# Kernel tuning notes

Hardware: AMD Instinct MI355X
Metric: run time of the kernel (lower is better)

## Reference

```python
import jax, jax.numpy as jnp
import numpy as np

B, H, O, T = 256, 1024, 512, 128


def setup_inputs() -> dict:
    key = jax.random.key(0)
    ks = jax.random.split(key, 7)
    s = 1.0 / np.sqrt(H)
    return {
        "C": jax.random.normal(ks[0], (B, H), jnp.float32),
        "W_ih": jax.random.normal(ks[1], (4 * H, H), jnp.float32) * s,
        "W_hh": jax.random.normal(ks[2], (4 * H, H), jnp.float32) * s,
        "b_ih": jax.random.normal(ks[3], (4 * H,), jnp.float32) * s,
        "b_hh": jax.random.normal(ks[4], (4 * H,), jnp.float32) * s,
        "W_lin": jax.random.normal(ks[5], (O, H), jnp.float32) * s,
        "b_lin": jax.random.normal(ks[6], (O,), jnp.float32) * s,
        "max_seq_len": T,
    }


def reference(C, W_ih, W_hh, b_ih, b_hh, W_lin, b_lin, max_seq_len):
    batch, hid = C.shape
    # Input is the same C at every timestep -> precompute input projection once.
    x_proj = C @ W_ih.T + b_ih + b_hh  # [B, 4H]

    def step(carry, _):
        h, c = carry
        gates = x_proj + h @ W_hh.T  # [B, 4H]
        i, f, g, o = jnp.split(gates, 4, axis=-1)  # torch gate order i,f,g,o
        i = jax.nn.sigmoid(i)
        f = jax.nn.sigmoid(f)
        g = jnp.tanh(g)
        o = jax.nn.sigmoid(o)
        c = f * c + i * g
        h = o * jnp.tanh(c)
        y = h @ W_lin.T + b_lin  # [B, O]
        return (h, c), y

    h0 = jnp.zeros((batch, hid), C.dtype)
    c0 = jnp.zeros((batch, hid), C.dtype)
    _, ys = jax.lax.scan(step, (h0, c0), None, length=max_seq_len)
    return ys  # [T, B, O]
```

## Files before the change

kernel.cpp:

```cpp
#include <hip/hip_runtime.h>

typedef _Float16 f16;
typedef _Float16 f16x4 __attribute__((ext_vector_type(4)));
typedef _Float16 f16x8 __attribute__((ext_vector_type(8)));
typedef float f32x2 __attribute__((ext_vector_type(2)));
typedef float f32x4 __attribute__((ext_vector_type(4)));

#define LSTM_B 256
#define LSTM_H 1024
#define LSTM_O 512
#define LSTM_T 128
#define GATES 4096


__global__ void cvt4_kernel(const float4* __restrict__ src, f16x4* __restrict__ dst, int n4) {
  int i = blockIdx.x * blockDim.x + threadIdx.x;
  int st = gridDim.x * blockDim.x;
  for (; i < n4; i += st) {
    float4 v = src[i];
    f16x4 o; o[0] = (f16)v.x; o[1] = (f16)v.y; o[2] = (f16)v.z; o[3] = (f16)v.w;
    dst[i] = o;
  }
}

__global__ void pack_whh_kernel(const float* __restrict__ Whh, f16* __restrict__ Wpack) {
  int idx = blockIdx.x * 256 + threadIdx.x;
  int lane = idx & 63;
  int f = (idx >> 6) & 127;
  int hj = idx >> 13;
  int kc = f >> 3, s = (f >> 2) & 1, wn = (f >> 1) & 1, nt = f & 1;
  int c = wn * 32 + nt * 16 + (lane & 15);
  int row = (c >> 4) * 1024 + hj * 16 + (c & 15);
  int k0 = kc * 64 + s * 32 + (lane >> 4) * 8;
  const float* src = Whh + (size_t)row * LSTM_H + k0;
  float4 v0 = *(const float4*)src;
  float4 v1 = *(const float4*)(src + 4);
  f16x8 o;
  o[0] = (f16)v0.x; o[1] = (f16)v0.y; o[2] = (f16)v0.z; o[3] = (f16)v0.w;
  o[4] = (f16)v1.x; o[5] = (f16)v1.y; o[6] = (f16)v1.z; o[7] = (f16)v1.w;
  *(f16x8*)(Wpack + (size_t)idx * 8) = o;
}

__global__ __launch_bounds__(256) void gemm_bt_kernel(
    const f16* __restrict__ A, const f16* __restrict__ Bw,
    const float* __restrict__ bias0, const float* __restrict__ bias1,
    float* __restrict__ out, int M, int N, int K, int gn, int xswz, int blkA)
{
  __shared__ __align__(16) f16 As[64][72];
  __shared__ __align__(16) f16 Bs[64][72];
  int bx = blockIdx.x;
  if (xswz) { int n = gridDim.x; bx = (bx & 7) * (n >> 3) + (bx >> 3); }
  int mb = bx / gn;
  int m0 = mb * 64;
  int n0 = (bx - mb * gn) * 64;
  int tid = threadIdx.x;
  int lane = tid & 63, w = tid >> 6;
  int wm = w >> 1, wn = w & 1;
  int sr = tid >> 2, sseg = tid & 3;
  const f16* ga;
  size_t kadv;
  if (blkA) {
    int m = m0 + sr;
    ga = A + ((size_t)(m >> 8) * 256 + (size_t)sseg * 4 + ((m >> 6) & 3)) * 1024 + (m & 63) * 16;
    kadv = 16384;
  } else {
    ga = A + (size_t)(m0 + sr) * K + sseg * 16;
    kadv = 64;
  }
  const f16* gb = Bw + (size_t)(n0 + sr) * K + sseg * 16;
  f32x4 acc00 = {}, acc01 = {}, acc10 = {}, acc11 = {};
  f16x8 ra0 = *(const f16x8*)ga, ra1 = *(const f16x8*)(ga + 8);
  f16x8 rb0 = *(const f16x8*)gb, rb1 = *(const f16x8*)(gb + 8);
  for (int kc = 0; kc < K; kc += 64) {
    __syncthreads();
    *(f16x8*)&As[sr][sseg * 16]     = ra0;
    *(f16x8*)&As[sr][sseg * 16 + 8] = ra1;
    *(f16x8*)&Bs[sr][sseg * 16]     = rb0;
    *(f16x8*)&Bs[sr][sseg * 16 + 8] = rb1;
    __syncthreads();
    if (kc + 64 < K) {
      ga += kadv; gb += 64;
      ra0 = *(const f16x8*)ga; ra1 = *(const f16x8*)(ga + 8);
      rb0 = *(const f16x8*)gb; rb1 = *(const f16x8*)(gb + 8);
    }
    int g = lane >> 4, r = lane & 15;
    #pragma unroll
    for (int s = 0; s < 2; s++) {
      f16x8 a0 = *(const f16x8*)&As[wm * 32      + r][s * 32 + g * 8];
      f16x8 a1 = *(const f16x8*)&As[wm * 32 + 16 + r][s * 32 + g * 8];
      f16x8 b0 = *(const f16x8*)&Bs[wn * 32      + r][s * 32 + g * 8];
      f16x8 b1 = *(const f16x8*)&Bs[wn * 32 + 16 + r][s * 32 + g * 8];
      acc00 = __builtin_amdgcn_mfma_f32_16x16x32_f16(a0, b0, acc00, 0, 0, 0);
      acc01 = __builtin_amdgcn_mfma_f32_16x16x32_f16(a0, b1, acc01, 0, 0, 0);
      acc10 = __builtin_amdgcn_mfma_f32_16x16x32_f16(a1, b0, acc10, 0, 0, 0);
      acc11 = __builtin_amdgcn_mfma_f32_16x16x32_f16(a1, b1, acc11, 0, 0, 0);
    }
  }
  int gq = lane >> 4, rr = lane & 15;
  f32x4 accs[2][2] = {{acc00, acc01}, {acc10, acc11}};
  #pragma unroll
  for (int mt = 0; mt < 2; mt++)
    #pragma unroll
    for (int nt = 0; nt < 2; nt++) {
      int row = m0 + wm * 32 + mt * 16 + gq * 4;
      int col = n0 + wn * 32 + nt * 16 + rr;
      float bv = bias0 ? bias0[col] : 0.f;
      if (bias1) bv += bias1[col];
      #pragma unroll
      for (int j = 0; j < 4; j++)
        out[(size_t)(row + j) * N + col] = accs[mt][nt][j] + bv;
    }
}

__global__ __launch_bounds__(256, 1) void lstm_persist_kernel(
    const f16* __restrict__ Wpack, const float* __restrict__ xp,
    f16* __restrict__ hist, unsigned* __restrict__ ready)
{
  __shared__ __align__(16) f16 Bres[65536];
  __shared__ float gsm[64][65];

  const int wg = blockIdx.x;
  const int mb = (wg & 7) >> 1;
  const int hj = ((wg >> 3) << 1) | (wg & 1);
  const int m0 = mb * 64;
  const int tid = threadIdx.x;
  const int lane = tid & 63, w = tid >> 6;
  const int g = lane >> 4, r = lane & 15;

  {
    const f16x8* src = (const f16x8*)(Wpack + (size_t)hj * 65536);
    f16x8* dst = (f16x8*)Bres;
    for (int i = tid; i < 8192; i += 256) dst[i] = src[i];
  }

  const int b_loc = tid & 63, hh0 = tid >> 6;
  const float* xprow = xp + (size_t)(m0 + b_loc) * GATES + hj * 16 + hh0 * 4;
  float4 xi = *(const float4*)(xprow);
  float4 xf = *(const float4*)(xprow + LSTM_H);
  float4 xg = *(const float4*)(xprow + 2 * LSTM_H);
  float4 xo = *(const float4*)(xprow + 3 * LSTM_H);
  float xiv[4] = {xi.x, xi.y, xi.z, xi.w};
  float xfv[4] = {xf.x, xf.y, xf.z, xf.w};
  float xgv[4] = {xg.x, xg.y, xg.z, xg.w};
  float xov[4] = {xo.x, xo.y, xo.z, xo.w};
  float cvv[4] = {0.f, 0.f, 0.f, 0.f};

  const int ainv = (g >> 1) * 4096 + mb * 1024 + w * 256 + r * 16 + (g & 1) * 8;
  const int stag = hj >> 2;
  const char* Bb0 = (const char*)Bres + lane * 16;
  f16* hob = hist + ((size_t)hj * 4 + mb) * 1024 + b_loc * 16 + hh0 * 4;

  __syncthreads();

  for (int t = 0; t < LSTM_T; t++) {
    f32x4 acc0 = {}, acc1 = {}, acc2 = {}, acc3 = {};
    if (t > 0) {
      const unsigned* flagp = ready + ((size_t)(t - 1) * 4 + mb) * 16;
      unsigned f;
      for (;;) {
        f = __hip_atomic_load(flagp, __ATOMIC_RELAXED, __HIP_MEMORY_SCOPE_AGENT);
        if (f >= 64u) break;
        __builtin_amdgcn_s_sleep(1);
      }
      const f16* hb = hist + (size_t)(t - 1) * 262144 + ainv + (f >> 7);
      f16x8 sa0[4], sa1[4];
      #pragma unroll
      for (int i = 0; i < 3; i++) {
        const int kc = (stag + i) & 15;
        sa0[i] = *(const f16x8*)(hb + kc * 16384);
        sa1[i] = *(const f16x8*)(hb + kc * 16384 + 8192);
      }
      #pragma unroll
      for (int i = 0; i < 16; i++) {
        const int kc = (stag + i) & 15;
        if (i + 3 < 16) {
          const int kn = (stag + i + 3) & 15;
          sa0[(i + 3) & 3] = *(const f16x8*)(hb + kn * 16384);
          sa1[(i + 3) & 3] = *(const f16x8*)(hb + kn * 16384 + 8192);
        }
        const char* Bb = Bb0 + kc * 8192;
        f16x8 b00 = *(const f16x8*)(Bb);
        f16x8 b01 = *(const f16x8*)(Bb + 1024);
        f16x8 b02 = *(const f16x8*)(Bb + 2048);
        f16x8 b03 = *(const f16x8*)(Bb + 3072);
        f16x8 b10 = *(const f16x8*)(Bb + 4096);
        f16x8 b11 = *(const f16x8*)(Bb + 5120);
        f16x8 b12 = *(const f16x8*)(Bb + 6144);
        f16x8 b13 = *(const f16x8*)(Bb + 7168);
        const f16x8 a0 = sa0[i & 3], a1 = sa1[i & 3];
        acc0 = __builtin_amdgcn_mfma_f32_16x16x32_f16(a0, b00, acc0, 0, 0, 0);
        acc1 = __builtin_amdgcn_mfma_f32_16x16x32_f16(a0, b01, acc1, 0, 0, 0);
        acc2 = __builtin_amdgcn_mfma_f32_16x16x32_f16(a0, b02, acc2, 0, 0, 0);
        acc3 = __builtin_amdgcn_mfma_f32_16x16x32_f16(a0, b03, acc3, 0, 0, 0);
        acc0 = __builtin_amdgcn_mfma_f32_16x16x32_f16(a1, b10, acc0, 0, 0, 0);
        acc1 = __builtin_amdgcn_mfma_f32_16x16x32_f16(a1, b11, acc1, 0, 0, 0);
        acc2 = __builtin_amdgcn_mfma_f32_16x16x32_f16(a1, b12, acc2, 0, 0, 0);
        acc3 = __builtin_amdgcn_mfma_f32_16x16x32_f16(a1, b13, acc3, 0, 0, 0);
      }
    }
    {
      f32x4 accs[4] = {acc0, acc1, acc2, acc3};
      #pragma unroll
      for (int n = 0; n < 4; n++)
        #pragma unroll
        for (int j = 0; j < 4; j++)
          gsm[w * 16 + g * 4 + j][n * 16 + r] = accs[n][j];
    }
    __syncthreads();
    float hnew[4];
    #pragma unroll
    for (int u = 0; u < 4; u++) {
      int hh = hh0 * 4 + u;
      float iv = gsm[b_loc][hh]      + xiv[u];
      float fv = gsm[b_loc][16 + hh] + xfv[u];
      float gv = gsm[b_loc][32 + hh] + xgv[u];
      float ov = gsm[b_loc][48 + hh] + xov[u];
      iv = 1.f / (1.f + __expf(-iv));
      fv = 1.f / (1.f + __expf(-fv));
      gv = 2.f / (1.f + __expf(-2.f * gv)) - 1.f;
      ov = 1.f / (1.f + __expf(-ov));
      float cn = fv * cvv[u] + iv * gv;
      cvv[u] = cn;
      float tc = 2.f / (1.f + __expf(-2.f * cn)) - 1.f;
      hnew[u] = ov * tc;
    }
    f16x4 hw; hw[0] = (f16)hnew[0]; hw[1] = (f16)hnew[1]; hw[2] = (f16)hnew[2]; hw[3] = (f16)hnew[3];
    {
      union { f16x4 h; f32x2 f2; } hu; hu.h = hw;
      f16* haddr = hob + (size_t)t * 262144;
      asm volatile("global_store_dwordx2 %0, %1, off sc0 sc1" :: "v"(haddr), "v"(hu.f2) : "memory");
    }
    if (t + 1 < LSTM_T) {
      asm volatile("s_waitcnt vmcnt(0)" ::: "memory");
      __syncthreads();
      if (tid == 0)
        __hip_atomic_fetch_add(ready + ((size_t)t * 4 + mb) * 16, 1u,
                               __ATOMIC_RELAXED, __HIP_MEMORY_SCOPE_AGENT);
    }
  }
}

extern "C" void kernel_launch(void* const* d_in, const int* in_sizes, int n_in,
                              void* d_out, int out_size, void* d_ws, size_t ws_size,
                              hipStream_t stream)
{
  (void)in_sizes; (void)n_in; (void)out_size; (void)ws_size;
  const float* C     = (const float*)d_in[0];
  const float* W_ih  = (const float*)d_in[1];
  const float* W_hh  = (const float*)d_in[2];
  const float* b_ih  = (const float*)d_in[3];
  const float* b_hh  = (const float*)d_in[4];
  const float* W_lin = (const float*)d_in[5];
  const float* b_lin = (const float*)d_in[6];

  char* ws = (char*)d_ws;
  size_t off = 0;
  auto alloc = [&](size_t bytes) { void* p = ws + off; off += (bytes + 255) & ~(size_t)255; return p; };
  f16*      Wih16  = (f16*)alloc((size_t)GATES * LSTM_H * 2);
  f16*      Wlin16 = (f16*)alloc((size_t)LSTM_O * LSTM_H * 2);
  f16*      C16    = (f16*)alloc((size_t)LSTM_B * LSTM_H * 2);
  f16*      Wpack  = (f16*)alloc((size_t)GATES * LSTM_H * 2);
  float*    xp     = (float*)alloc((size_t)LSTM_B * GATES * 4);
  f16*      hist   = (f16*)alloc((size_t)LSTM_T * LSTM_B * LSTM_H * 2);
  unsigned* ready  = (unsigned*)alloc((size_t)LSTM_T * 4 * 16 * 4);

  cvt4_kernel<<<2048, 256, 0, stream>>>((const float4*)W_ih,  (f16x4*)Wih16,  GATES * LSTM_H / 4);
  cvt4_kernel<<<512,  256, 0, stream>>>((const float4*)W_lin, (f16x4*)Wlin16, LSTM_O * LSTM_H / 4);
  cvt4_kernel<<<256,  256, 0, stream>>>((const float4*)C,     (f16x4*)C16,    LSTM_B * LSTM_H / 4);
  pack_whh_kernel<<<2048, 256, 0, stream>>>(W_hh, Wpack);
  hipMemsetAsync(ready, 0, (size_t)LSTM_T * 4 * 16 * 4, stream);

  gemm_bt_kernel<<<(LSTM_B / 64) * (GATES / 64), 256, 0, stream>>>(
      C16, Wih16, b_ih, b_hh, xp, LSTM_B, GATES, LSTM_H, GATES / 64, 0, 0);

  {
    const f16* wp = Wpack; const float* xpp = xp; f16* hp = hist; unsigned* rp = ready;
    void* args[] = { (void*)&wp, (void*)&xpp, (void*)&hp, (void*)&rp };
    hipLaunchCooperativeKernel((void*)lstm_persist_kernel, dim3(256), dim3(256), args, 0, stream);
  }

  gemm_bt_kernel<<<(LSTM_T * LSTM_B / 64) * (LSTM_O / 64), 256, 0, stream>>>(
      hist, Wlin16, b_lin, nullptr, (float*)d_out,
      LSTM_T * LSTM_B, LSTM_O, LSTM_H, LSTM_O / 64, 1, 1);
}
```

Measured before the change: 1.066 ms.

## Compute LSTM cell directly from MFMA accumulators and use per-chunk readiness flags

Each wave now computes the gate nonlinearities directly from its MFMA accumulator layout. This removes the shared-memory gate transpose and its block barrier, and the x-projection values are preloaded in the matching layout. Readiness signalling moves from one counter per batch block to one counter per K-chunk, bumped per wave. Consumers then wait only for the specific chunk they are about to load, so dependency waits overlap with the MFMA loop. The cost is scattered 2-byte h stores in place of 8-byte ones, and 16 flag loads per step.

After: 1.264 ms. 1.19x slower.

```diff
diff --git a/kernel.cpp b/kernel.cpp
--- a/kernel.cpp
+++ b/kernel.cpp
@@ -117,7 +117,6 @@
     f16* __restrict__ hist, unsigned* __restrict__ ready)
 {
   __shared__ __align__(16) f16 Bres[65536];
-  __shared__ float gsm[64][65];
 
   const int wg = blockIdx.x;
   const int mb = (wg & 7) >> 1;
@@ -133,50 +132,59 @@
     for (int i = tid; i < 8192; i += 256) dst[i] = src[i];
   }
 
-  const int b_loc = tid & 63, hh0 = tid >> 6;
-  const float* xprow = xp + (size_t)(m0 + b_loc) * GATES + hj * 16 + hh0 * 4;
-  float4 xi = *(const float4*)(xprow);
-  float4 xf = *(const float4*)(xprow + LSTM_H);
-  float4 xg = *(const float4*)(xprow + 2 * LSTM_H);
-  float4 xo = *(const float4*)(xprow + 3 * LSTM_H);
-  float xiv[4] = {xi.x, xi.y, xi.z, xi.w};
-  float xfv[4] = {xf.x, xf.y, xf.z, xf.w};
-  float xgv[4] = {xg.x, xg.y, xg.z, xg.w};
-  float xov[4] = {xo.x, xo.y, xo.z, xo.w};
+  float xpv[4][4];
+  #pragma unroll
+  for (int j = 0; j < 4; j++) {
+    const float* row = xp + (size_t)(m0 + w * 16 + g * 4 + j) * GATES + hj * 16 + r;
+    #pragma unroll
+    for (int n = 0; n < 4; n++) xpv[n][j] = row[n * 1024];
+  }
   float cvv[4] = {0.f, 0.f, 0.f, 0.f};
 
   const int ainv = (g >> 1) * 4096 + mb * 1024 + w * 256 + r * 16 + (g & 1) * 8;
   const int stag = hj >> 2;
   const char* Bb0 = (const char*)Bres + lane * 16;
-  f16* hob = hist + ((size_t)hj * 4 + mb) * 1024 + b_loc * 16 + hh0 * 4;
+  f16* hb_out = hist + (size_t)hj * 4096 + (size_t)mb * 1024
+              + (size_t)(w * 16 + g * 4) * 16 + r;
 
   __syncthreads();
 
   for (int t = 0; t < LSTM_T; t++) {
     f32x4 acc0 = {}, acc1 = {}, acc2 = {}, acc3 = {};
     if (t > 0) {
-      const unsigned* flagp = ready + ((size_t)(t - 1) * 4 + mb) * 16;
-      unsigned f;
-      for (;;) {
-        f = __hip_atomic_load(flagp, __ATOMIC_RELAXED, __HIP_MEMORY_SCOPE_AGENT);
-        if (f >= 64u) break;
-        __builtin_amdgcn_s_sleep(1);
-      }
-      const f16* hb = hist + (size_t)(t - 1) * 262144 + ainv + (f >> 7);
+      const unsigned* rdt = ready + ((size_t)(t - 1) * 4 + mb) * 256;
+      unsigned fv[16];
+      #pragma unroll
+      for (int j = 0; j < 16; j++)
+        fv[j] = __hip_atomic_load(rdt + ((stag + j) & 15) * 16,
+                                  __ATOMIC_RELAXED, __HIP_MEMORY_SCOPE_AGENT);
+      const f16* hb = hist + (size_t)(t - 1) * 262144 + ainv;
       f16x8 sa0[4], sa1[4];
       #pragma unroll
-      for (int i = 0; i < 3; i++) {
-        const int kc = (stag + i) & 15;
-        sa0[i] = *(const f16x8*)(hb + kc * 16384);
-        sa1[i] = *(const f16x8*)(hb + kc * 16384 + 8192);
+      for (int j = 0; j < 3; j++) {
+        const int kc = (stag + j) & 15;
+        unsigned f = fv[j];
+        while (f < 16u) {
+          __builtin_amdgcn_s_sleep(1);
+          f = __hip_atomic_load(rdt + kc * 16, __ATOMIC_RELAXED, __HIP_MEMORY_SCOPE_AGENT);
+        }
+        const f16* p = hb + kc * 16384 + (f >> 5);
+        sa0[j] = *(const f16x8*)p;
+        sa1[j] = *(const f16x8*)(p + 8192);
       }
       #pragma unroll
       for (int i = 0; i < 16; i++) {
         const int kc = (stag + i) & 15;
         if (i + 3 < 16) {
           const int kn = (stag + i + 3) & 15;
-          sa0[(i + 3) & 3] = *(const f16x8*)(hb + kn * 16384);
-          sa1[(i + 3) & 3] = *(const f16x8*)(hb + kn * 16384 + 8192);
+          unsigned f = fv[i + 3];
+          while (f < 16u) {
+            __builtin_amdgcn_s_sleep(1);
+            f = __hip_atomic_load(rdt + kn * 16, __ATOMIC_RELAXED, __HIP_MEMORY_SCOPE_AGENT);
+          }
+          const f16* p = hb + kn * 16384 + (f >> 5);
+          sa0[(i + 3) & 3] = *(const f16x8*)p;
+          sa1[(i + 3) & 3] = *(const f16x8*)(p + 8192);
         }
         const char* Bb = Bb0 + kc * 8192;
         f16x8 b00 = *(const f16x8*)(Bb);
@@ -198,43 +206,34 @@
         acc3 = __builtin_amdgcn_mfma_f32_16x16x32_f16(a1, b13, acc3, 0, 0, 0);
       }
     }
-    {
-      f32x4 accs[4] = {acc0, acc1, acc2, acc3};
-      #pragma unroll
-      for (int n = 0; n < 4; n++)
-        #pragma unroll
-        for (int j = 0; j < 4; j++)
-          gsm[w * 16 + g * 4 + j][n * 16 + r] = accs[n][j];
-    }
-    __syncthreads();
-    float hnew[4];
-    #pragma unroll
-    for (int u = 0; u < 4; u++) {
-      int hh = hh0 * 4 + u;
-      float iv = gsm[b_loc][hh]      + xiv[u];
-      float fv = gsm[b_loc][16 + hh] + xfv[u];
-      float gv = gsm[b_loc][32 + hh] + xgv[u];
-      float ov = gsm[b_loc][48 + hh] + xov[u];
+    float hn[4];
+    #pragma unroll
+    for (int j = 0; j < 4; j++) {
+      float iv = acc0[j] + xpv[0][j];
+      float fg = acc1[j] + xpv[1][j];
+      float gv = acc2[j] + xpv[2][j];
+      float ov = acc3[j] + xpv[3][j];
       iv = 1.f / (1.f + __expf(-iv));
-      fv = 1.f / (1.f + __expf(-fv));
+      fg = 1.f / (1.f + __expf(-fg));
       gv = 2.f / (1.f + __expf(-2.f * gv)) - 1.f;
       ov = 1.f / (1.f + __expf(-ov));
-      float cn = fv * cvv[u] + iv * gv;
-      cvv[u] = cn;
-      float tc = 2.f / (1.f + __expf(-2.f * cn)) - 1.f;
-      hnew[u] = ov * tc;
-    }
-    f16x4 hw; hw[0] = (f16)hnew[0]; hw[1] = (f16)hnew[1]; hw[2] = (f16)hnew[2]; hw[3] = (f16)hnew[3];
+      float cn = fg * cvv[j] + iv * gv;
+      cvv[j] = cn;
+      hn[j] = ov * (2.f / (1.f + __expf(-2.f * cn)) - 1.f);
+    }
     {
-      union { f16x4 h; f32x2 f2; } hu; hu.h = hw;
-      f16* haddr = hob + (size_t)t * 262144;
-      asm volatile("global_store_dwordx2 %0, %1, off sc0 sc1" :: "v"(haddr), "v"(hu.f2) : "memory");
+      f16* ha = hb_out + (size_t)t * 262144;
+      union { f16 h; unsigned short u; } u0, u1, u2, u3;
+      u0.h = (f16)hn[0]; u1.h = (f16)hn[1]; u2.h = (f16)hn[2]; u3.h = (f16)hn[3];
+      asm volatile("global_store_short %0, %1, off sc0 sc1"            :: "v"(ha), "v"((unsigned)u0.u) : "memory");
+      asm volatile("global_store_short %0, %1, off offset:32 sc0 sc1"  :: "v"(ha), "v"((unsigned)u1.u) : "memory");
+      asm volatile("global_store_short %0, %1, off offset:64 sc0 sc1"  :: "v"(ha), "v"((unsigned)u2.u) : "memory");
+      asm volatile("global_store_short %0, %1, off offset:96 sc0 sc1"  :: "v"(ha), "v"((unsigned)u3.u) : "memory");
     }
     if (t + 1 < LSTM_T) {
       asm volatile("s_waitcnt vmcnt(0)" ::: "memory");
-      __syncthreads();
-      if (tid == 0)
-        __hip_atomic_fetch_add(ready + ((size_t)t * 4 + mb) * 16, 1u,
+      if (lane == 0)
+        __hip_atomic_fetch_add(ready + (((size_t)t * 4 + mb) * 16 + stag) * 16, 1u,
                                __ATOMIC_RELAXED, __HIP_MEMORY_SCOPE_AGENT);
     }
   }
@@ -262,13 +261,13 @@
   f16*      Wpack  = (f16*)alloc((size_t)GATES * LSTM_H * 2);
   float*    xp     = (float*)alloc((size_t)LSTM_B * GATES * 4);
   f16*      hist   = (f16*)alloc((size_t)LSTM_T * LSTM_B * LSTM_H * 2);
-  unsigned* ready  = (unsigned*)alloc((size_t)LSTM_T * 4 * 16 * 4);
+  unsigned* ready  = (unsigned*)alloc((size_t)LSTM_T * 4 * 16 * 16 * 4);
 
   cvt4_kernel<<<2048, 256, 0, stream>>>((const float4*)W_ih,  (f16x4*)Wih16,  GATES * LSTM_H / 4);
   cvt4_kernel<<<512,  256, 0, stream>>>((const float4*)W_lin, (f16x4*)Wlin16, LSTM_O * LSTM_H / 4);
   cvt4_kernel<<<256,  256, 0, stream>>>((const float4*)C,     (f16x4*)C16,    LSTM_B * LSTM_H / 4);
   pack_whh_kernel<<<2048, 256, 0, stream>>>(W_hh, Wpack);
-  hipMemsetAsync(ready, 0, (size_t)LSTM_T * 4 * 16 * 4, stream);
+  hipMemsetAsync(ready, 0, (size_t)LSTM_T * 4 * 16 * 16 * 4, stream);
 
   gemm_bt_kernel<<<(LSTM_B / 64) * (GATES / 64), 256, 0, stream>>>(
       C16, Wih16, b_ih, b_hh, xp, LSTM_B, GATES, LSTM_H, GATES / 64, 0, 0);
```
